# Kernel tuning notes

Measured on AMD Instinct MI355X. Metric: run time of the kernel, lower is better.

## Reference

```python
import jax, jax.numpy as jnp
import numpy as np

GRID_SIZE = 5
SPLINE_ORDER = 3
N_COEFFS = GRID_SIZE + SPLINE_ORDER  # 8
N_KNOTS = N_COEFFS + SPLINE_ORDER    # 11
GRID_RANGE = 5.0
# extended knot grid: linspace(-9, 9, 11) for the defaults
_lo = -GRID_RANGE - (SPLINE_ORDER - 1) * 2.0 * GRID_RANGE / GRID_SIZE
_hi = GRID_RANGE + (SPLINE_ORDER - 1) * 2.0 * GRID_RANGE / GRID_SIZE
GRID = jnp.asarray(np.linspace(_lo, _hi, N_KNOTS), dtype=jnp.float32)


def _bspline_basis(x):
    # x: (B, I) -> basis: (B, I, N_COEFFS) via Cox-de Boor recursion
    xe = x[..., None]  # (B, I, 1)
    # order-1 (piecewise-constant) basis over the 10 knot intervals
    bases = ((xe >= GRID[:-1]) & (xe < GRID[1:])).astype(x.dtype)  # (B, I, 10)
    for k in range(1, SPLINE_ORDER):
        n = N_KNOTS - k - 1  # number of bases at this order
        g_i = GRID[:n]
        g_ik = GRID[k:k + n]
        g_i1 = GRID[1:n + 1]
        g_ik1 = GRID[k + 1:k + 1 + n]
        d1 = g_ik - g_i
        d2 = g_ik1 - g_i1
        left = jnp.where(d1 > 1e-8, (xe - g_i) / jnp.where(d1 > 1e-8, d1, 1.0), 0.0) * bases[..., :n]
        right = jnp.where(d2 > 1e-8, (g_ik1 - xe) / jnp.where(d2 > 1e-8, d2, 1.0), 0.0) * bases[..., 1:n + 1]
        bases = left + right
    return bases  # (B, I, 8)


def setup_inputs() -> dict:
    key = jax.random.key(0)
    k1, k2, k3 = jax.random.split(key, 3)
    B, I, O = 8192, 1024, 1024
    x = jax.random.normal(k1, (B, I), dtype=jnp.float32)
    base_weight = jax.random.normal(k2, (O, I), dtype=jnp.float32) * 0.1
    spline_weight = jax.random.normal(k3, (O, I, N_COEFFS), dtype=jnp.float32) * 0.1
    return {"x": x, "base_weight": base_weight, "spline_weight": spline_weight}


def reference(x, base_weight, spline_weight):
    base_out = jnp.einsum('bi,oi->bo', jax.nn.silu(x), base_weight)
    basis = _bspline_basis(x)  # (B, I, 8)
    spline_out = jnp.einsum('bin,oin->bo', basis, spline_weight)
    return base_out + spline_out
```

## Files before the change

kernel.cpp:

```cpp
#include <hip/hip_runtime.h>
#include <hip/hip_bf16.h>

#define B_DIM 8192
#define I_DIM 1024
#define O_DIM 1024
#define K_DIM 9216

#define BM 256
#define BN 256
#define BK 64

typedef unsigned short ushort_t;
typedef __attribute__((ext_vector_type(8))) short short8;
typedef __attribute__((ext_vector_type(4))) float f32x4;

#define MFMA(a, b, c) __builtin_amdgcn_mfma_f32_16x16x32_bf16((a), (b), (c), 0, 0, 0)

__device__ __forceinline__ ushort_t f2bf(float f) {
    unsigned u = __float_as_uint(f);
    unsigned r = 0x7fffu + ((u >> 16) & 1u);
    return (ushort_t)((u + r) >> 16);
}

__device__ __forceinline__ void llds16(const ushort_t* g, ushort_t* l) {
    __builtin_amdgcn_global_load_lds(
        (const __attribute__((address_space(1))) unsigned int*)g,
        (__attribute__((address_space(3))) unsigned int*)l,
        16, 0, 0);
}

__global__ __launch_bounds__(256) void expand_w_kernel(
        const float* __restrict__ bw, const float* __restrict__ sw,
        ushort_t* __restrict__ Wf) {
    int idx = blockIdx.x * 256 + threadIdx.x;
    int o = idx >> 9;
    int i = (idx & 511) << 1;
    ushort_t* out = Wf + (size_t)o * K_DIM + i;
    const float* bp = bw + ((size_t)o << 10) + i;
    *(unsigned*)out = (unsigned)f2bf(bp[0]) | ((unsigned)f2bf(bp[1]) << 16);
    const float* sp = sw + (((size_t)o << 10) + i) * 8;
    float v[16];
    #pragma unroll
    for (int n = 0; n < 16; ++n) v[n] = sp[n];
    #pragma unroll
    for (int n = 0; n < 8; ++n)
        *(unsigned*)(out + (size_t)(n + 1) * 1024) =
            (unsigned)f2bf(v[n]) | ((unsigned)f2bf(v[8 + n]) << 16);
}

__global__ __launch_bounds__(256) void expand_a_kernel(
        const float* __restrict__ x, ushort_t* __restrict__ Af) {
    int idx = blockIdx.x * 256 + threadIdx.x;
    int b = idx >> 9;
    int i = (idx & 511) << 1;
    const float* xp = x + ((size_t)b << 10) + i;
    float x0 = xp[0], x1 = xp[1];
    ushort_t* out = Af + (size_t)b * K_DIM + i;
    float s0 = x0 / (1.0f + __expf(-x0));
    float s1 = x1 / (1.0f + __expf(-x1));
    *(unsigned*)out = (unsigned)f2bf(s0) | ((unsigned)f2bf(s1) << 16);
    float t0 = (x0 + 9.0f) * (1.0f / 1.8f);
    float t1 = (x1 + 9.0f) * (1.0f / 1.8f);
    float fj0 = floorf(t0), fj1 = floorf(t1);
    int j0 = (int)fj0, j1 = (int)fj1;
    float u0 = t0 - fj0, u1 = t1 - fj1;
    float p0 = 0.5f * (1.f - u0) * (1.f - u0);
    float p1 = 0.5f * (-2.f * u0 * u0 + 2.f * u0 + 1.f);
    float p2 = 0.5f * u0 * u0;
    float q0 = 0.5f * (1.f - u1) * (1.f - u1);
    float q1 = 0.5f * (-2.f * u1 * u1 + 2.f * u1 + 1.f);
    float q2 = 0.5f * u1 * u1;
    #pragma unroll
    for (int n = 0; n < 8; ++n) {
        float v0 = (n == j0 - 2) ? p0 : (n == j0 - 1) ? p1 : (n == j0) ? p2 : 0.f;
        float v1 = (n == j1 - 2) ? q0 : (n == j1 - 1) ? q1 : (n == j1) ? q2 : 0.f;
        *(unsigned*)(out + (size_t)(n + 1) * 1024) =
            (unsigned)f2bf(v0) | ((unsigned)f2bf(v1) << 16);
    }
}

__global__ __launch_bounds__(512, 1) void gemm_bt(
        const ushort_t* __restrict__ Af,
        const ushort_t* __restrict__ Wf,
        float* __restrict__ out, float* __restrict__ part1,
        int kTiles) {
    __shared__ __align__(16) ushort_t As[3][BM * BK];
    __shared__ __align__(16) ushort_t Bs[2][BN * BK];

    const int tid = threadIdx.x;

    const int nwg = gridDim.x;
    const int orig = blockIdx.x;
    const int wgid = (orig & 7) * (nwg >> 3) + (orig >> 3);
    const int split = wgid >> 7;
    const int bm = (wgid & 127) >> 2;
    const int bn = wgid & 3;
    const int mBase = bm * BM, nBase = bn * BN;
    const size_t kOff = (size_t)split * kTiles * BK;

    const int lane = tid & 63;
    const int w = tid >> 6;
    const int wr = (w >> 2) * 128;
    const int wc = (w & 3) * 64;
    const int fr = lane & 15;
    const int kg = lane >> 4;

    const int srow = tid >> 3;
    const int scolE = (((tid & 7) ^ (srow & 7)) << 3);
    const int sdst = (tid & ~63) * 8;

    auto stageA = [&](int t, int buf, int rnd) {
        const ushort_t* g = Af + (size_t)(mBase + rnd * 64 + srow) * K_DIM
                               + kOff + (size_t)t * BK + scolE;
        llds16(g, &As[buf][rnd * 4096 + sdst]);
    };
    auto stageB = [&](int t, int buf, int rnd) {
        const ushort_t* g = Wf + (size_t)(nBase + rnd * 64 + srow) * K_DIM
                               + kOff + (size_t)t * BK + scolE;
        llds16(g, &Bs[buf][rnd * 4096 + sdst]);
    };

    const int swz0 = ((kg ^ (fr & 7)) << 3);
    const int swz1 = (((4 + kg) ^ (fr & 7)) << 3);

    f32x4 acc[8][4];
    #pragma unroll
    for (int m = 0; m < 8; ++m)
        #pragma unroll
        for (int n = 0; n < 4; ++n) acc[m][n] = (f32x4){0.f, 0.f, 0.f, 0.f};

    auto tile_body = [&](int t, int ca, int pa, bool doB, bool doA) {
        const ushort_t* A_ = As[ca];
        const ushort_t* B_ = Bs[t & 1];
        short8 a[4][2], b0[2][2], b1[2][2];

        #pragma unroll
        for (int m = 0; m < 4; ++m) {
            int arow = (wr + m * 16 + fr) * BK;
            a[m][0] = *(const short8*)&A_[arow + swz0];
            a[m][1] = *(const short8*)&A_[arow + swz1];
        }
        #pragma unroll
        for (int n = 0; n < 2; ++n) {
            int brow = (wc + n * 16 + fr) * BK;
            b0[n][0] = *(const short8*)&B_[brow + swz0];
            b0[n][1] = *(const short8*)&B_[brow + swz1];
        }
        asm volatile("s_waitcnt lgkmcnt(0)" ::: "memory");
        __builtin_amdgcn_sched_barrier(0);
        __builtin_amdgcn_s_setprio(1);
        #pragma unroll
        for (int m = 0; m < 4; ++m)
            #pragma unroll
            for (int n = 0; n < 2; ++n) {
                acc[m][n] = MFMA(a[m][0], b0[n][0], acc[m][n]);
                acc[m][n] = MFMA(a[m][1], b0[n][1], acc[m][n]);
            }
        __builtin_amdgcn_s_setprio(0);
        __builtin_amdgcn_s_barrier();

        if (doB) {
            stageB(t + 1, (t + 1) & 1, 0); stageB(t + 1, (t + 1) & 1, 1);
            stageB(t + 1, (t + 1) & 1, 2); stageB(t + 1, (t + 1) & 1, 3);
        }
        #pragma unroll
        for (int n = 0; n < 2; ++n) {
            int brow = (wc + (2 + n) * 16 + fr) * BK;
            b1[n][0] = *(const short8*)&B_[brow + swz0];
            b1[n][1] = *(const short8*)&B_[brow + swz1];
        }
        asm volatile("s_waitcnt lgkmcnt(0)" ::: "memory");
        __builtin_amdgcn_sched_barrier(0);
        __builtin_amdgcn_s_setprio(1);
        #pragma unroll
        for (int m = 0; m < 4; ++m)
            #pragma unroll
            for (int n = 0; n < 2; ++n) {
                acc[m][2 + n] = MFMA(a[m][0], b1[n][0], acc[m][2 + n]);
                acc[m][2 + n] = MFMA(a[m][1], b1[n][1], acc[m][2 + n]);
            }
        __builtin_amdgcn_s_setprio(0);
        __builtin_amdgcn_s_barrier();

        #pragma unroll
        for (int m = 0; m < 4; ++m) {
            int arow = (wr + (4 + m) * 16 + fr) * BK;
            a[m][0] = *(const short8*)&A_[arow + swz0];
            a[m][1] = *(const short8*)&A_[arow + swz1];
        }
        asm volatile("s_waitcnt lgkmcnt(0)" ::: "memory");
        __builtin_amdgcn_sched_barrier(0);
        __builtin_amdgcn_s_setprio(1);
        #pragma unroll
        for (int m = 0; m < 4; ++m)
            #pragma unroll
            for (int n = 0; n < 2; ++n) {
                acc[4 + m][n] = MFMA(a[m][0], b0[n][0], acc[4 + m][n]);
                acc[4 + m][n] = MFMA(a[m][1], b0[n][1], acc[4 + m][n]);
            }
        __builtin_amdgcn_s_setprio(0);
        __builtin_amdgcn_s_barrier();

        if (doA) {
            stageA(t + 2, pa, 0); stageA(t + 2, pa, 1);
            stageA(t + 2, pa, 2); stageA(t + 2, pa, 3);
        }
        __builtin_amdgcn_s_setprio(1);
        #pragma unroll
        for (int m = 0; m < 4; ++m)
            #pragma unroll
            for (int n = 0; n < 2; ++n) {
                acc[4 + m][2 + n] = MFMA(a[m][0], b1[n][0], acc[4 + m][2 + n]);
                acc[4 + m][2 + n] = MFMA(a[m][1], b1[n][1], acc[4 + m][2 + n]);
            }
        __builtin_amdgcn_s_setprio(0);
    };

    stageB(0, 0, 0); stageB(0, 0, 1); stageB(0, 0, 2); stageB(0, 0, 3);
    stageA(0, 0, 0); stageA(0, 0, 1); stageA(0, 0, 2); stageA(0, 0, 3);
    stageA(1, 1, 0); stageA(1, 1, 1); stageA(1, 1, 2); stageA(1, 1, 3);

    int ca = 0;
    for (int t = 0; t < kTiles - 1; ++t) {
        asm volatile("s_waitcnt vmcnt(4)" ::: "memory");
        __builtin_amdgcn_s_barrier();
        const int pa = (ca >= 1) ? ca - 1 : 2;
        tile_body(t, ca, pa, true, t + 2 < kTiles);
        ca = (ca + 1 == 3) ? 0 : ca + 1;
    }
    {
        const int t = kTiles - 1;
        asm volatile("s_waitcnt vmcnt(0)" ::: "memory");
        __builtin_amdgcn_s_barrier();
        tile_body(t, ca, 0, false, false);
    }

    float* obase = split ? part1 : out;
    const int orow = (lane >> 4) * 4;
    const int ocol = lane & 15;
    #pragma unroll
    for (int m = 0; m < 8; ++m)
        #pragma unroll
        for (int n = 0; n < 4; ++n) {
            size_t base = (size_t)(mBase + wr + m * 16 + orow) * O_DIM
                        + (nBase + wc + n * 16 + ocol);
            #pragma unroll
            for (int r = 0; r < 4; ++r)
                obase[base + (size_t)r * O_DIM] = acc[m][n][r];
        }
}

__global__ __launch_bounds__(256) void reduce_kernel(
        float* __restrict__ out, const float* __restrict__ p1) {
    int i = blockIdx.x * 256 + threadIdx.x;
    f32x4 a = ((const f32x4*)out)[i];
    f32x4 b = ((const f32x4*)p1)[i];
    ((f32x4*)out)[i] = a + b;
}

extern "C" void kernel_launch(void* const* d_in, const int* in_sizes, int n_in,
                              void* d_out, int out_size, void* d_ws, size_t ws_size,
                              hipStream_t stream) {
    const float* x  = (const float*)d_in[0];
    const float* bw = (const float*)d_in[1];
    const float* sw = (const float*)d_in[2];
    float* out = (float*)d_out;

    const size_t nW = (size_t)O_DIM * K_DIM;
    const size_t nA = (size_t)B_DIM * K_DIM;
    ushort_t* Wf = (ushort_t*)d_ws;
    ushort_t* Af = Wf + nW;
    float* part1 = (float*)(Af + nA);
    const size_t need = (nW + nA) * 2 + (size_t)B_DIM * O_DIM * 4;

    const int nsplit = (ws_size >= need) ? 2 : 1;
    const int kTiles = (K_DIM / BK) / nsplit;
    const int nwg = 128 * nsplit;

    expand_w_kernel<<<(O_DIM * I_DIM / 2) / 256, 256, 0, stream>>>(bw, sw, Wf);
    expand_a_kernel<<<(B_DIM * I_DIM / 2) / 256, 256, 0, stream>>>(x, Af);
    gemm_bt<<<nwg, 512, 0, stream>>>(Af, Wf, out, part1, kTiles);
    if (nsplit == 2)
        reduce_kernel<<<(B_DIM * O_DIM / 4) / 256, 256, 0, stream>>>(out, part1);
}
```

Before: 212.9 us.

## Restructure GEMM main loop with single barrier and rolling A-fragment prefetch

Rewrites the K-loop so each tile issues all global-to-LDS staging for the next tiles up front after one barrier. It then loads all B fragments once and streams A fragments through three rotating register buffers, using partial lgkmcnt waits so LDS reads overlap MFMAs. The four intra-tile barriers are removed and launch_bounds min-blocks is dropped. The trade-off is that the loop now waits on vmcnt(0) every tile instead of vmcnt(4), which may expose more global-load latency.

```diff
diff --git a/kernel.cpp b/kernel.cpp
--- a/kernel.cpp
+++ b/kernel.cpp
@@ -79,7 +79,7 @@
     }
 }
 
-__global__ __launch_bounds__(512, 1) void gemm_bt(
+__global__ __launch_bounds__(512) void gemm_bt(
         const ushort_t* __restrict__ Af,
         const ushort_t* __restrict__ Wf,
         float* __restrict__ out, float* __restrict__ part1,
@@ -109,15 +109,21 @@
     const int scolE = (((tid & 7) ^ (srow & 7)) << 3);
     const int sdst = (tid & ~63) * 8;
 
-    auto stageA = [&](int t, int buf, int rnd) {
-        const ushort_t* g = Af + (size_t)(mBase + rnd * 64 + srow) * K_DIM
-                               + kOff + (size_t)t * BK + scolE;
-        llds16(g, &As[buf][rnd * 4096 + sdst]);
-    };
-    auto stageB = [&](int t, int buf, int rnd) {
-        const ushort_t* g = Wf + (size_t)(nBase + rnd * 64 + srow) * K_DIM
-                               + kOff + (size_t)t * BK + scolE;
-        llds16(g, &Bs[buf][rnd * 4096 + sdst]);
+    auto stageA = [&](int t, int buf) {
+        #pragma unroll
+        for (int rnd = 0; rnd < 4; ++rnd) {
+            const ushort_t* g = Af + (size_t)(mBase + rnd * 64 + srow) * K_DIM
+                                   + kOff + (size_t)t * BK + scolE;
+            llds16(g, &As[buf][rnd * 4096 + sdst]);
+        }
+    };
+    auto stageB = [&](int t, int buf) {
+        #pragma unroll
+        for (int rnd = 0; rnd < 4; ++rnd) {
+            const ushort_t* g = Wf + (size_t)(nBase + rnd * 64 + srow) * K_DIM
+                                   + kOff + (size_t)t * BK + scolE;
+            llds16(g, &Bs[buf][rnd * 4096 + sdst]);
+        }
     };
 
     const int swz0 = ((kg ^ (fr & 7)) << 3);
@@ -129,110 +135,71 @@
         #pragma unroll
         for (int n = 0; n < 4; ++n) acc[m][n] = (f32x4){0.f, 0.f, 0.f, 0.f};
 
-    auto tile_body = [&](int t, int ca, int pa, bool doB, bool doA) {
+    short8 b[4][2];
+    short8 F0[2][2], F1[2][2], F2[2][2];
+
+    auto ldA = [&](short8 (&F)[2][2], const ushort_t* A_, int m0) {
+        #pragma unroll
+        for (int i = 0; i < 2; ++i) {
+            int arow = (wr + (m0 + i) * 16 + fr) * BK;
+            F[i][0] = *(const short8*)&A_[arow + swz0];
+            F[i][1] = *(const short8*)&A_[arow + swz1];
+        }
+    };
+    auto mm16 = [&](short8 (&F)[2][2], int p) {
+        __builtin_amdgcn_s_setprio(1);
+        #pragma unroll
+        for (int i = 0; i < 2; ++i)
+            #pragma unroll
+            for (int n = 0; n < 4; ++n) {
+                acc[2 * p + i][n] = MFMA(F[i][0], b[n][0], acc[2 * p + i][n]);
+                acc[2 * p + i][n] = MFMA(F[i][1], b[n][1], acc[2 * p + i][n]);
+            }
+        __builtin_amdgcn_s_setprio(0);
+    };
+
+    stageB(0, 0);
+    stageA(0, 0);
+    stageA(1, 1);
+
+    int ca = 0;
+    for (int t = 0; t < kTiles; ++t) {
         const ushort_t* A_ = As[ca];
         const ushort_t* B_ = Bs[t & 1];
-        short8 a[4][2], b0[2][2], b1[2][2];
-
-        #pragma unroll
-        for (int m = 0; m < 4; ++m) {
-            int arow = (wr + m * 16 + fr) * BK;
-            a[m][0] = *(const short8*)&A_[arow + swz0];
-            a[m][1] = *(const short8*)&A_[arow + swz1];
-        }
-        #pragma unroll
-        for (int n = 0; n < 2; ++n) {
-            int brow = (wc + n * 16 + fr) * BK;
-            b0[n][0] = *(const short8*)&B_[brow + swz0];
-            b0[n][1] = *(const short8*)&B_[brow + swz1];
-        }
-        asm volatile("s_waitcnt lgkmcnt(0)" ::: "memory");
-        __builtin_amdgcn_sched_barrier(0);
-        __builtin_amdgcn_s_setprio(1);
-        #pragma unroll
-        for (int m = 0; m < 4; ++m)
-            #pragma unroll
-            for (int n = 0; n < 2; ++n) {
-                acc[m][n] = MFMA(a[m][0], b0[n][0], acc[m][n]);
-                acc[m][n] = MFMA(a[m][1], b0[n][1], acc[m][n]);
-            }
-        __builtin_amdgcn_s_setprio(0);
-        __builtin_amdgcn_s_barrier();
-
-        if (doB) {
-            stageB(t + 1, (t + 1) & 1, 0); stageB(t + 1, (t + 1) & 1, 1);
-            stageB(t + 1, (t + 1) & 1, 2); stageB(t + 1, (t + 1) & 1, 3);
-        }
-        #pragma unroll
-        for (int n = 0; n < 2; ++n) {
-            int brow = (wc + (2 + n) * 16 + fr) * BK;
-            b1[n][0] = *(const short8*)&B_[brow + swz0];
-            b1[n][1] = *(const short8*)&B_[brow + swz1];
-        }
-        asm volatile("s_waitcnt lgkmcnt(0)" ::: "memory");
-        __builtin_amdgcn_sched_barrier(0);
-        __builtin_amdgcn_s_setprio(1);
-        #pragma unroll
-        for (int m = 0; m < 4; ++m)
-            #pragma unroll
-            for (int n = 0; n < 2; ++n) {
-                acc[m][2 + n] = MFMA(a[m][0], b1[n][0], acc[m][2 + n]);
-                acc[m][2 + n] = MFMA(a[m][1], b1[n][1], acc[m][2 + n]);
-            }
-        __builtin_amdgcn_s_setprio(0);
-        __builtin_amdgcn_s_barrier();
-
-        #pragma unroll
-        for (int m = 0; m < 4; ++m) {
-            int arow = (wr + (4 + m) * 16 + fr) * BK;
-            a[m][0] = *(const short8*)&A_[arow + swz0];
-            a[m][1] = *(const short8*)&A_[arow + swz1];
-        }
-        asm volatile("s_waitcnt lgkmcnt(0)" ::: "memory");
-        __builtin_amdgcn_sched_barrier(0);
-        __builtin_amdgcn_s_setprio(1);
-        #pragma unroll
-        for (int m = 0; m < 4; ++m)
-            #pragma unroll
-            for (int n = 0; n < 2; ++n) {
-                acc[4 + m][n] = MFMA(a[m][0], b0[n][0], acc[4 + m][n]);
-                acc[4 + m][n] = MFMA(a[m][1], b0[n][1], acc[4 + m][n]);
-            }
-        __builtin_amdgcn_s_setprio(0);
-        __builtin_amdgcn_s_barrier();
-
-        if (doA) {
-            stageA(t + 2, pa, 0); stageA(t + 2, pa, 1);
-            stageA(t + 2, pa, 2); stageA(t + 2, pa, 3);
-        }
-        __builtin_amdgcn_s_setprio(1);
-        #pragma unroll
-        for (int m = 0; m < 4; ++m)
-            #pragma unroll
-            for (int n = 0; n < 2; ++n) {
-                acc[4 + m][2 + n] = MFMA(a[m][0], b1[n][0], acc[4 + m][2 + n]);
-                acc[4 + m][2 + n] = MFMA(a[m][1], b1[n][1], acc[4 + m][2 + n]);
-            }
-        __builtin_amdgcn_s_setprio(0);
-    };
-
-    stageB(0, 0, 0); stageB(0, 0, 1); stageB(0, 0, 2); stageB(0, 0, 3);
-    stageA(0, 0, 0); stageA(0, 0, 1); stageA(0, 0, 2); stageA(0, 0, 3);
-    stageA(1, 1, 0); stageA(1, 1, 1); stageA(1, 1, 2); stageA(1, 1, 3);
-
-    int ca = 0;
-    for (int t = 0; t < kTiles - 1; ++t) {
-        asm volatile("s_waitcnt vmcnt(4)" ::: "memory");
-        __builtin_amdgcn_s_barrier();
         const int pa = (ca >= 1) ? ca - 1 : 2;
-        tile_body(t, ca, pa, true, t + 2 < kTiles);
-        ca = (ca + 1 == 3) ? 0 : ca + 1;
-    }
-    {
-        const int t = kTiles - 1;
+
         asm volatile("s_waitcnt vmcnt(0)" ::: "memory");
         __builtin_amdgcn_s_barrier();
-        tile_body(t, ca, 0, false, false);
+        __builtin_amdgcn_sched_barrier(0);
+        if (t + 1 < kTiles) stageB(t + 1, (t + 1) & 1);
+        if (t + 2 < kTiles) stageA(t + 2, pa);
+        #pragma unroll
+        for (int n = 0; n < 4; ++n) {
+            int brow = (wc + n * 16 + fr) * BK;
+            b[n][0] = *(const short8*)&B_[brow + swz0];
+            b[n][1] = *(const short8*)&B_[brow + swz1];
+        }
+        ldA(F0, A_, 0);
+        ldA(F1, A_, 2);
+        asm volatile("s_waitcnt lgkmcnt(4)" ::: "memory");
+        __builtin_amdgcn_sched_barrier(0);
+        mm16(F0, 0);
+
+        ldA(F2, A_, 4);
+        asm volatile("s_waitcnt lgkmcnt(4)" ::: "memory");
+        __builtin_amdgcn_sched_barrier(0);
+        mm16(F1, 1);
+
+        ldA(F0, A_, 6);
+        asm volatile("s_waitcnt lgkmcnt(4)" ::: "memory");
+        __builtin_amdgcn_sched_barrier(0);
+        mm16(F2, 2);
+
+        asm volatile("s_waitcnt lgkmcnt(0)" ::: "memory");
+        __builtin_amdgcn_sched_barrier(0);
+        mm16(F0, 3);
+
+        ca = (ca + 1 == 3) ? 0 : ca + 1;
     }
 
     float* obase = split ? part1 : out;
```

Result: faster. 205.1 us (-3.6%).
